# Kernel optimization log

Hardware: AMD Instinct MI355X
Metric: run time of the kernel (lower is better)

The kernel has to match this reference:

```python
import jax, jax.numpy as jnp
import numpy as np

N = 50000   # nodes
E = 600000  # edges
D = 128     # in_feats == n_hidden


def setup_inputs() -> dict:
    key = jax.random.key(0)
    ks = jax.random.split(key, 10)
    s = 0.1
    return {
        "x": jax.random.normal(ks[0], (N, D), jnp.float32),
        "W1": jax.random.normal(ks[1], (D, D), jnp.float32) * s,
        "b1": jnp.zeros((D,), jnp.float32),
        "W2": jax.random.normal(ks[2], (D, D), jnp.float32) * s,
        "b2": jnp.zeros((D,), jnp.float32),
        "Wp": jax.random.normal(ks[3], (D, D), jnp.float32) * s,
        "bp": jnp.zeros((D,), jnp.float32),
        "edge_src": jax.random.randint(ks[4], (E,), 0, N),
        "edge_dst": jax.random.randint(ks[5], (E,), 0, N),
        "perm": jax.random.randint(ks[6], (N,), 0, N),
    }


def _graph_conv(h, W, b, src, dst, norm):
    # DGL GraphConv (norm='both'): D^-1/2 A D^-1/2 H W + b
    m = h[src] * norm[src, None]                      # [E, D] gather
    agg = jax.ops.segment_sum(m, dst, num_segments=N)  # [N, D] scatter-add
    return (agg * norm[:, None]) @ W + b


def _encode(x, W1, b1, W2, b2, src, dst, norm):
    h = jax.nn.relu(_graph_conv(x, W1, b1, src, dst, norm))
    return _graph_conv(h, W2, b2, src, dst, norm)


def reference(x, W1, b1, W2, b2, Wp, bp, edge_src, edge_dst, perm):
    # symmetric normalization from in-degree (clamped to avoid div by 0)
    deg = jax.ops.segment_sum(jnp.ones((E,), x.dtype), edge_dst, num_segments=N)
    norm = jax.lax.rsqrt(jnp.maximum(deg, 1.0))

    h1 = _encode(x, W1, b1, W2, b2, edge_src, edge_dst, norm)        # clean
    h2 = _encode(x[perm], W1, b1, W2, b2, edge_src, edge_dst, norm)  # corrupt

    sc1 = (h1 @ Wp + bp).sum(axis=1)  # [N]
    sc2 = (h2 @ Wp + bp).sum(axis=1)  # [N]

    logits = jnp.concatenate([sc1, sc2])                   # [2N]
    lbl = jnp.concatenate([jnp.ones((N,), x.dtype), jnp.zeros((N,), x.dtype)])
    # BCEWithLogitsLoss (mean): softplus(z) - z*y  (numerically stable)
    loss = jnp.mean(jax.nn.softplus(logits) - logits * lbl)
    return loss
```

## Files before the change

### kernel.cpp

```cpp
#include <hip/hip_runtime.h>
#include <math.h>

#define D 128

typedef float f32x2 __attribute__((ext_vector_type(2)));

__device__ __forceinline__ float softplusf(float z){
    return log1pf(expf(-fabsf(z))) + fmaxf(z, 0.f);
}

__global__ void __launch_bounds__(256) k_fused1(
    const float* __restrict__ x, const float* __restrict__ W1,
    unsigned* __restrict__ xw8, int N,
    const int* __restrict__ edst, int* __restrict__ deg, int E,
    int nGemm,
    const float* __restrict__ W2, const float* __restrict__ b2,
    const float* __restrict__ Wp, const float* __restrict__ bp,
    float* __restrict__ v, float* __restrict__ cconst)
{
    __shared__ float smem[32*D + 32*36];
    const int b = blockIdx.x;
    const int tid = threadIdx.x;
    if (b == 0){
        float* wps = smem;
        int lane = tid & 63, wid = tid >> 6;
        for (int r = wid; r < D; r += 4){
            float a = Wp[(size_t)r*D + lane] + Wp[(size_t)r*D + 64 + lane];
            for (int off=32; off>0; off>>=1) a += __shfl_down(a, off);
            if (lane == 0) wps[r] = a;
        }
        __syncthreads();
        float wl0 = wps[lane], wl1 = wps[64 + lane];
        for (int r = wid; r < D; r += 4){
            float a = W2[(size_t)r*D + lane]*wl0 + W2[(size_t)r*D + 64 + lane]*wl1;
            for (int off=32; off>0; off>>=1) a += __shfl_down(a, off);
            if (lane == 0) v[r] = a;
        }
        if (wid == 0){
            float a = b2[lane]*wl0 + b2[64+lane]*wl1 + bp[lane] + bp[64+lane];
            for (int off=32; off>0; off>>=1) a += __shfl_down(a, off);
            if (lane == 0) cconst[0] = a;
        }
    } else if (b <= nGemm){
        float* Ws = smem;
        float (*xs)[36] = (float(*)[36])(smem + 32*D);
        const int cg = tid & 31;
        const int rg = tid >> 5;
        int row0 = (b - 1) * 32;
        float4 acc[4];
        #pragma unroll
        for (int q=0;q<4;q++) acc[q] = make_float4(0.f,0.f,0.f,0.f);
        for (int p = 0; p < 4; ++p){
            int k0 = p*32;
            {
                int r = tid >> 5;
                int c = (tid & 31) * 4;
                #pragma unroll
                for (int s2 = 0; s2 < 4; ++s2){
                    int kk = r + s2*8;
                    *(float4*)&Ws[kk*D + c] = *(const float4*)&W1[(size_t)(k0+kk)*D + c];
                }
            }
            {
                int rr = tid >> 3;
                int cc = (tid & 7) * 4;
                int grow = row0 + rr;
                float4 vx = make_float4(0.f,0.f,0.f,0.f);
                if (grow < N) vx = *(const float4*)&x[(size_t)grow*D + k0 + cc];
                *(float4*)&xs[rr][cc] = vx;
            }
            __syncthreads();
            #pragma unroll
            for (int kk = 0; kk < 32; ++kk){
                float4 w = *(const float4*)&Ws[kk*D + cg*4];
                #pragma unroll
                for (int q = 0; q < 4; ++q){
                    float xv = xs[rg*4 + q][kk];
                    acc[q].x = fmaf(xv, w.x, acc[q].x);
                    acc[q].y = fmaf(xv, w.y, acc[q].y);
                    acc[q].z = fmaf(xv, w.z, acc[q].z);
                    acc[q].w = fmaf(xv, w.w, acc[q].w);
                }
            }
            __syncthreads();
        }
        #pragma unroll
        for (int q = 0; q < 4; ++q){
            int r = row0 + rg*4 + q;
            if (r < N){
                unsigned lo = (unsigned)__builtin_amdgcn_cvt_pk_fp8_f32(acc[q].x, acc[q].y, 0, false);
                unsigned u  = (unsigned)__builtin_amdgcn_cvt_pk_fp8_f32(acc[q].z, acc[q].w, (int)lo, true);
                xw8[(size_t)r*32 + cg] = u;
            }
        }
    } else {
        int e = (b - nGemm - 1)*256 + tid;
        if (e < E) atomicAdd(&deg[edst[e]], 1);
    }
}

__global__ void k_scanA(const int* __restrict__ deg, int* __restrict__ offs,
                        int* __restrict__ bsum, int N){
    __shared__ int wsums[16];
    __shared__ int gtot;
    int tid = threadIdx.x, lane = tid & 63, wid = tid >> 6;
    int g = blockIdx.x*1024 + tid;
    int val = (g < N) ? deg[g] : 0;
    int inc = val;
    #pragma unroll
    for (int off=1; off<64; off<<=1){
        int t = __shfl_up(inc, off);
        if (lane >= off) inc += t;
    }
    if (lane == 63) wsums[wid] = inc;
    __syncthreads();
    if (wid == 0 && lane < 16){
        int t = wsums[lane];
        int i2 = t;
        #pragma unroll
        for (int off=1; off<16; off<<=1){
            int u = __shfl_up(i2, off);
            if (lane >= off) i2 += u;
        }
        wsums[lane] = i2 - t;
        if (lane == 15) gtot = i2;
    }
    __syncthreads();
    if (g < N) offs[g] = wsums[wid] + inc - val;
    if (tid == 0) bsum[blockIdx.x] = gtot;
}

__global__ void k_scanC(int* __restrict__ offs, const int* __restrict__ bsum,
                        int* __restrict__ cursor, const int* __restrict__ deg,
                        float* __restrict__ norm, int2* __restrict__ ep,
                        const int* __restrict__ perm, int N){
    __shared__ int sbase;
    int tid = threadIdx.x;
    if (tid < 64){
        int val = (tid < (int)blockIdx.x) ? bsum[tid] : 0;
        for (int off=32; off>0; off>>=1) val += __shfl_down(val, off);
        if (tid == 0) sbase = val;
    }
    __syncthreads();
    int g = blockIdx.x*1024 + tid;
    if (g < N){
        int o = offs[g] + sbase;
        offs[g] = o;
        cursor[g] = o;
        float nm = rsqrtf(fmaxf((float)deg[g], 1.f));
        norm[g] = nm;
        ep[g] = make_int2(perm[g], __float_as_int(nm));
    }
}

__global__ void k_fill(const int* __restrict__ src, const int* __restrict__ dst,
                       int* __restrict__ cursor, unsigned short* __restrict__ csr, int E){
    int e = blockIdx.x*blockDim.x + threadIdx.x;
    if (e < E){
        int dd = dst[e];
        int p = atomicAdd(&cursor[dd], 1);
        csr[p] = (unsigned short)src[e];
    }
}

#define FMA8(u, nk) { \
    f32x2 f01 = __builtin_amdgcn_cvt_pk_f32_fp8((int)(u), false); \
    f32x2 f23 = __builtin_amdgcn_cvt_pk_f32_fp8((int)(u), true);  \
    ac.x = fmaf(f01.x, (nk), ac.x); ac.y = fmaf(f01.y, (nk), ac.y); \
    ac.z = fmaf(f23.x, (nk), ac.z); ac.w = fmaf(f23.y, (nk), ac.w); }

__global__ void __launch_bounds__(256) k_agg(const unsigned* __restrict__ xw8,
                     const unsigned short* __restrict__ csr, const int* __restrict__ offs,
                     const int* __restrict__ deg, const float* __restrict__ norm,
                     const int2* __restrict__ ep, const float* __restrict__ b1,
                     const float* __restrict__ v, float2* __restrict__ t2, int N){
    int w = threadIdx.x >> 6;
    int lane = threadIdx.x & 63;
    int i = blockIdx.x*4 + w;
    if (i >= N) return;
    int half = lane >> 5;
    int c = lane & 31;
    const unsigned* __restrict__ xr = xw8;
    float4 ac = make_float4(0.f,0.f,0.f,0.f);
    int start = offs[i], cnt = deg[i];

    for (int base = 0; base < cnt; base += 64){
        int m = min(cnt - base, 64);
        int s = 0, sp = 0; float ns = 0.f;
        if (lane < m){
            s = csr[start + base + lane];
            int2 e = ep[s];
            sp = e.x; ns = __int_as_float(e.y);
        }
        int k = 0;
        for (; k + 4 <= m; k += 4){
            int ra0=__shfl(s,k  ), rb0=__shfl(sp,k  ); float n0=__shfl(ns,k  );
            int ra1=__shfl(s,k+1), rb1=__shfl(sp,k+1); float n1=__shfl(ns,k+1);
            int ra2=__shfl(s,k+2), rb2=__shfl(sp,k+2); float n2=__shfl(ns,k+2);
            int ra3=__shfl(s,k+3), rb3=__shfl(sp,k+3); float n3=__shfl(ns,k+3);
            int r0 = half ? rb0 : ra0;
            int r1 = half ? rb1 : ra1;
            int r2 = half ? rb2 : ra2;
            int r3 = half ? rb3 : ra3;
            unsigned d0 = xr[(size_t)r0*32 + c];
            unsigned d1 = xr[(size_t)r1*32 + c];
            unsigned d2 = xr[(size_t)r2*32 + c];
            unsigned d3 = xr[(size_t)r3*32 + c];
            FMA8(d0, n0); FMA8(d1, n1); FMA8(d2, n2); FMA8(d3, n3);
        }
        for (; k < m; ++k){
            int ra=__shfl(s,k), rb=__shfl(sp,k); float nk=__shfl(ns,k);
            int r = half ? rb : ra;
            unsigned dv = xr[(size_t)r*32 + c];
            FMA8(dv, nk);
        }
    }
    float ni = norm[i];
    float4 bb = ((const float4*)b1)[c];
    float4 vv = ((const float4*)v)[c];
    float p = fmaxf(fmaf(ac.x, ni, bb.x), 0.f)*vv.x
            + fmaxf(fmaf(ac.y, ni, bb.y), 0.f)*vv.y
            + fmaxf(fmaf(ac.z, ni, bb.z), 0.f)*vv.z
            + fmaxf(fmaf(ac.w, ni, bb.w), 0.f)*vv.w;
    for (int off=16; off>0; off>>=1) p += __shfl_xor(p, off);
    float pd = __shfl(p, 32);
    if (lane == 0) t2[i] = make_float2(ni*p, ni*pd);
}

__global__ void k_loss(const float2* __restrict__ t2, const unsigned short* __restrict__ csr,
                       const int* __restrict__ offs, const int* __restrict__ deg,
                       const float* __restrict__ norm, const float* __restrict__ cconst,
                       float* __restrict__ acc, unsigned* __restrict__ done,
                       float* __restrict__ out, int N, int nblocks){
    int i = blockIdx.x*blockDim.x + threadIdx.x;
    float li = 0.f;
    if (i < N){
        int start = offs[i], cnt = deg[i];
        float sc = 0.f, sd = 0.f;
        for (int k=0;k<cnt;k++){
            int s = csr[start+k];
            float2 t = t2[s];
            sc += t.x; sd += t.y;
        }
        float ni = norm[i], C = cconst[0];
        li = softplusf(-fmaf(ni, sc, C)) + softplusf(fmaf(ni, sd, C));
    }
    for (int off=32; off>0; off>>=1) li += __shfl_down(li, off);
    __shared__ float wsum[4];
    int lane = threadIdx.x & 63, wid = threadIdx.x >> 6;
    if (lane == 0) wsum[wid] = li;
    __syncthreads();
    if (threadIdx.x == 0){
        float s = wsum[0] + wsum[1] + wsum[2] + wsum[3];
        atomicAdd(acc, s);
        __threadfence();
        unsigned t = atomicAdd(done, 1u);
        if (t == (unsigned)(nblocks - 1)){
            float tot = atomicAdd(acc, 0.0f);
            out[0] = tot / (float)(2*N);
        }
    }
}

extern "C" void kernel_launch(void* const* d_in, const int* in_sizes, int n_in,
                              void* d_out, int out_size, void* d_ws, size_t ws_size,
                              hipStream_t stream){
    const float* x    = (const float*)d_in[0];
    const float* W1   = (const float*)d_in[1];
    const float* b1   = (const float*)d_in[2];
    const float* W2   = (const float*)d_in[3];
    const float* b2   = (const float*)d_in[4];
    const float* Wp   = (const float*)d_in[5];
    const float* bp   = (const float*)d_in[6];
    const int*   esrc = (const int*)d_in[7];
    const int*   edst = (const int*)d_in[8];
    const int*   perm = (const int*)d_in[9];
    const int N = in_sizes[0] / D;
    const int E = in_sizes[7];

    char* ws = (char*)d_ws;
    size_t off = 0;
    auto alloc = [&](size_t bytes)->void*{
        void* p = ws + off;
        off += (bytes + 255) & ~(size_t)255;
        return p;
    };
    unsigned* xw8 = (unsigned*)alloc((size_t)N*32*sizeof(unsigned));
    int*   deg    = (int*)  alloc((size_t)N*sizeof(int));
    float* norm   = (float*)alloc((size_t)N*sizeof(float));
    int*   offs   = (int*)  alloc((size_t)N*sizeof(int));
    int*   cursor = (int*)  alloc((size_t)N*sizeof(int));
    int2*  ep     = (int2*) alloc((size_t)N*sizeof(int2));
    unsigned short* csr = (unsigned short*)alloc((size_t)E*sizeof(unsigned short));
    float2* t2    = (float2*)alloc((size_t)N*sizeof(float2));
    int*   bsum   = (int*)  alloc(4096);
    float* v      = (float*)alloc(D*sizeof(float));
    float* cconst = (float*)alloc(256);
    float* acc    = (float*)alloc(256);
    unsigned* done = (unsigned*)(acc + 1);

    hipMemsetAsync(deg, 0, (size_t)N*sizeof(int), stream);
    hipMemsetAsync(acc, 0, 256, stream);

    int nGemm = (N + 31) / 32;
    int nDeg  = (E + 255) / 256;
    int nb    = (N + 1023) / 1024;
    int nLoss = (N + 255) / 256;

    k_fused1<<<1 + nGemm + nDeg, 256, 0, stream>>>(x, W1, xw8, N, edst, deg, E,
                                                   nGemm, W2, b2, Wp, bp, v, cconst);
    k_scanA<<<nb, 1024, 0, stream>>>(deg, offs, bsum, N);
    k_scanC<<<nb, 1024, 0, stream>>>(offs, bsum, cursor, deg, norm, ep, perm, N);
    k_fill <<<(E+255)/256, 256, 0, stream>>>(esrc, edst, cursor, csr, E);
    k_agg  <<<(N+3)/4, 256, 0, stream>>>(xw8, csr, offs, deg, norm, ep, b1, v, t2, N);
    k_loss <<<nLoss, 256, 0, stream>>>(t2, csr, offs, deg, norm, cconst, acc, done,
                                       (float*)d_out, N, nLoss);
}
```

Baseline: 147.3 us.

## Compute x@W1 with bf16 MFMA instead of scalar FMA tiles

Replaces the fp32 FMA shared-memory GEMM in the fused first kernel with bf16 MFMA 16x16x32 instructions. Each block now handles 64 rows, with W1 transposed into an XOR-swizzled bf16 shared buffer and x loaded straight into registers. This is meant to cut the compute cost of the x·W1 projection. In exchange, every block reconverts the whole W1, bf16 input rounding adds error, and the output is written as scattered byte stores rather than packed 32-bit words.

```diff
diff --git a/kernel.cpp b/kernel.cpp
--- a/kernel.cpp
+++ b/kernel.cpp
@@ -4,9 +4,19 @@
 #define D 128
 
 typedef float f32x2 __attribute__((ext_vector_type(2)));
+typedef float f32x4 __attribute__((ext_vector_type(4)));
+typedef short short8 __attribute__((ext_vector_type(8)));
 
 __device__ __forceinline__ float softplusf(float z){
     return log1pf(expf(-fabsf(z))) + fmaxf(z, 0.f);
+}
+__device__ __forceinline__ unsigned short f2bf(float f){
+    unsigned u = __float_as_uint(f);
+    u += 0x7fffu + ((u >> 16) & 1u);
+    return (unsigned short)(u >> 16);
+}
+__device__ __forceinline__ int wt_idx(int row, int k){
+    return row*128 + ((((k >> 3) ^ (row & 7)) << 3) | (k & 7));
 }
 
 __global__ void __launch_bounds__(256) k_fused1(
@@ -18,11 +28,12 @@
     const float* __restrict__ Wp, const float* __restrict__ bp,
     float* __restrict__ v, float* __restrict__ cconst)
 {
-    __shared__ float smem[32*D + 32*36];
+    __shared__ unsigned short Wt[128*128];
+    __shared__ float pres[128];
     const int b = blockIdx.x;
     const int tid = threadIdx.x;
     if (b == 0){
-        float* wps = smem;
+        float* wps = pres;
         int lane = tid & 63, wid = tid >> 6;
         for (int r = wid; r < D; r += 4){
             float a = Wp[(size_t)r*D + lane] + Wp[(size_t)r*D + 64 + lane];
@@ -42,55 +53,56 @@
             if (lane == 0) cconst[0] = a;
         }
     } else if (b <= nGemm){
-        float* Ws = smem;
-        float (*xs)[36] = (float(*)[36])(smem + 32*D);
-        const int cg = tid & 31;
-        const int rg = tid >> 5;
-        int row0 = (b - 1) * 32;
-        float4 acc[4];
+        const int l = tid & 63, w = tid >> 6;
+        const int row0 = (b - 1) * 64;
+        #pragma unroll 8
+        for (int p = 0; p < 64; ++p){
+            int ic = p & 15;
+            int ik = (p >> 4) + w*4;
+            int c = ic*8 + (l & 7);
+            int k = ik*8 + (l >> 3);
+            Wt[wt_idx(c, k)] = f2bf(W1[(size_t)k*D + c]);
+        }
+        int arow = row0 + w*16 + (l & 15);
+        int kbase = (l >> 4) * 8;
+        short8 a[4];
         #pragma unroll
-        for (int q=0;q<4;q++) acc[q] = make_float4(0.f,0.f,0.f,0.f);
-        for (int p = 0; p < 4; ++p){
-            int k0 = p*32;
-            {
-                int r = tid >> 5;
-                int c = (tid & 31) * 4;
-                #pragma unroll
-                for (int s2 = 0; s2 < 4; ++s2){
-                    int kk = r + s2*8;
-                    *(float4*)&Ws[kk*D + c] = *(const float4*)&W1[(size_t)(k0+kk)*D + c];
-                }
+        for (int kc = 0; kc < 4; ++kc){
+            float4 f0 = make_float4(0.f,0.f,0.f,0.f), f1 = f0;
+            if (arow < N){
+                const float* px = &x[(size_t)arow*D + kc*32 + kbase];
+                f0 = *(const float4*)px;
+                f1 = *(const float4*)(px + 4);
             }
-            {
-                int rr = tid >> 3;
-                int cc = (tid & 7) * 4;
-                int grow = row0 + rr;
-                float4 vx = make_float4(0.f,0.f,0.f,0.f);
-                if (grow < N) vx = *(const float4*)&x[(size_t)grow*D + k0 + cc];
-                *(float4*)&xs[rr][cc] = vx;
+            short8 av;
+            av[0]=(short)f2bf(f0.x); av[1]=(short)f2bf(f0.y);
+            av[2]=(short)f2bf(f0.z); av[3]=(short)f2bf(f0.w);
+            av[4]=(short)f2bf(f1.x); av[5]=(short)f2bf(f1.y);
+            av[6]=(short)f2bf(f1.z); av[7]=(short)f2bf(f1.w);
+            a[kc] = av;
+        }
+        __syncthreads();
+        int colg = (l & 15);
+        #pragma unroll
+        for (int nt = 0; nt < 8; ++nt){
+            int col = nt*16 + colg;
+            short8 bq[4];
+            #pragma unroll
+            for (int kc = 0; kc < 4; ++kc){
+                int k0 = kc*32 + kbase;
+                bq[kc] = *(const short8*)&Wt[wt_idx(col, k0)];
             }
-            __syncthreads();
+            f32x4 acc = {0.f, 0.f, 0.f, 0.f};
             #pragma unroll
-            for (int kk = 0; kk < 32; ++kk){
-                float4 w = *(const float4*)&Ws[kk*D + cg*4];
-                #pragma unroll
-                for (int q = 0; q < 4; ++q){
-                    float xv = xs[rg*4 + q][kk];
-                    acc[q].x = fmaf(xv, w.x, acc[q].x);
-                    acc[q].y = fmaf(xv, w.y, acc[q].y);
-                    acc[q].z = fmaf(xv, w.z, acc[q].z);
-                    acc[q].w = fmaf(xv, w.w, acc[q].w);
-                }
-            }
-            __syncthreads();
-        }
-        #pragma unroll
-        for (int q = 0; q < 4; ++q){
-            int r = row0 + rg*4 + q;
-            if (r < N){
-                unsigned lo = (unsigned)__builtin_amdgcn_cvt_pk_fp8_f32(acc[q].x, acc[q].y, 0, false);
-                unsigned u  = (unsigned)__builtin_amdgcn_cvt_pk_fp8_f32(acc[q].z, acc[q].w, (int)lo, true);
-                xw8[(size_t)r*32 + cg] = u;
+            for (int kc = 0; kc < 4; ++kc)
+                acc = __builtin_amdgcn_mfma_f32_16x16x32_bf16(a[kc], bq[kc], acc, 0, 0, 0);
+            int rbase = row0 + w*16 + (l >> 4)*4;
+            #pragma unroll
+            for (int rp = 0; rp < 2; ++rp){
+                int pk = __builtin_amdgcn_cvt_pk_fp8_f32(acc[rp*2], acc[rp*2+1], 0, false);
+                int r0 = rbase + rp*2;
+                if (r0 < N)     ((unsigned char*)xw8)[(size_t)r0*D + col]     = (unsigned char)(pk & 0xff);
+                if (r0 + 1 < N) ((unsigned char*)xw8)[(size_t)(r0+1)*D + col] = (unsigned char)((pk >> 8) & 0xff);
             }
         }
     } else {
@@ -302,7 +314,7 @@
     hipMemsetAsync(deg, 0, (size_t)N*sizeof(int), stream);
     hipMemsetAsync(acc, 0, 256, stream);
 
-    int nGemm = (N + 31) / 32;
+    int nGemm = (N + 63) / 64;
     int nDeg  = (E + 255) / 256;
     int nb    = (N + 1023) / 1024;
     int nLoss = (N + 255) / 256;
```

Result: faster. 138.1 us (-6.3%).
